# Kernel tuning notes

Measured on AMD Instinct MI355X. Metric: run time of the kernel, lower is better.

## Reference

```python
import jax, jax.numpy as jnp
import numpy as np


def _maxpool2x2(t):
    # t: [B, C, H, W] -> [B, C, H//2, W//2]
    B, C, H, W = t.shape
    return t.reshape(B, C, H // 2, 2, W // 2, 2).max(axis=(3, 5))


def setup_inputs() -> dict:
    key = jax.random.key(0)
    ks = jax.random.split(key, 6)
    B, C, H, W = 2, 64, 128, 128
    x = jax.random.normal(ks[0], (B, C, H, W), dtype=jnp.float32)
    w_theta = jax.random.normal(ks[1], (C // 8, C), dtype=jnp.float32) * 0.05
    w_phi = jax.random.normal(ks[2], (C // 8, C), dtype=jnp.float32) * 0.05
    w_g = jax.random.normal(ks[3], (C // 2, C), dtype=jnp.float32) * 0.05
    w_o = jax.random.normal(ks[4], (C, C // 2), dtype=jnp.float32) * 0.05
    gamma = jnp.ones((1,), dtype=jnp.float32)
    return {"x": x, "w_theta": w_theta, "w_phi": w_phi, "w_g": w_g,
            "w_o": w_o, "gamma": gamma}


def reference(x, w_theta, w_phi, w_g, w_o, gamma):
    B, C, H, W = x.shape
    N = H * W            # query length
    M = (H // 2) * (W // 2)  # downsampled key/value length

    # conv1x1 projections (kernel_size=1 == per-pixel matmul over channels)
    theta = jnp.einsum('bchw,oc->bohw', x, w_theta).reshape(B, C // 8, N)
    phi = jnp.einsum('bchw,oc->bohw', x, w_phi)
    phi = _maxpool2x2(phi).reshape(B, C // 8, M)

    # attention: [B, N, M], unscaled dot product + softmax over keys
    attn = jax.nn.softmax(jnp.einsum('bdn,bdm->bnm', theta, phi), axis=-1)

    g = jnp.einsum('bchw,oc->bohw', x, w_g)
    g = _maxpool2x2(g).reshape(B, C // 2, M)

    attn_g = jnp.einsum('bcm,bnm->bcn', g, attn).reshape(B, C // 2, H, W)
    attn_g = jnp.einsum('bchw,oc->bohw', attn_g, w_o)
    return x + gamma * attn_g
```

## Files before the change

kernel.cpp:

```cpp
#include <hip/hip_runtime.h>

#define BB 2
#define CC 64
#define HH 128
#define WW 128
#define NN (HH*WW)
#define MM ((HH/2)*(WW/2))
#define CV 32
#define LOG2E 1.44269504088896f

typedef __attribute__((ext_vector_type(8))) short bf16x8;
typedef __attribute__((ext_vector_type(4))) float f32x4;
typedef unsigned int uint32;

union U8 { bf16x8 v; uint32 u[4]; };

__device__ __forceinline__ short f2bf(float f) {
    union { float f; unsigned u; } v; v.f = f;
    unsigned u = v.u + 0x7fffu + ((v.u >> 16) & 1u);
    return (short)(u >> 16);
}
__device__ __forceinline__ uint32 pack2bf(float lo, float hi) {
    return (uint32)(unsigned short)f2bf(lo) | ((uint32)(unsigned short)f2bf(hi) << 16);
}
__device__ __forceinline__ uint32 packperm(float lo, float hi) {
    union { float f; uint32 u; } a, b; a.f = lo; b.f = hi;
    return __builtin_amdgcn_perm(b.u, a.u, 0x07060302u);
}
__device__ __forceinline__ void gl_lds16(const short* g, short* l) {
    __builtin_amdgcn_global_load_lds(
        (const __attribute__((address_space(1))) void*)g,
        (__attribute__((address_space(3))) void*)l, 16, 0, 0);
}

__global__ __launch_bounds__(256, 4) void proj_kernel(
    const float* __restrict__ x, const float* __restrict__ wt,
    const float* __restrict__ wp, const float* __restrict__ wg,
    short* __restrict__ Qb, short* __restrict__ Kb, short* __restrict__ Vt)
{
    __shared__ float plds[8192];
    __shared__ float phi_lds[512];
    int tid = threadIdx.x;
    int px = tid & 63, part = tid >> 6;
    int sb = blockIdx.x >> 2, cq = blockIdx.x & 3;
    int b = blockIdx.y, z = blockIdx.z;
    int row = px >> 5, col = cq*32 + (px & 31);
    int n = (2*sb + row)*WW + col;
    int wbase = __builtin_amdgcn_readfirstlane(part*16);

    float xv[16];
    #pragma unroll
    for (int i = 0; i < 16; ++i)
        xv[i] = x[((b*CC + part*16 + i) << 14) + n];

    if (z == 0) {
        float po[16];
        #pragma unroll
        for (int o = 0; o < 8; ++o) {
            float a = 0.f;
            #pragma unroll
            for (int i = 0; i < 16; ++i) a += wt[o*64 + wbase + i]*xv[i];
            po[o] = a;
        }
        #pragma unroll
        for (int o = 0; o < 8; ++o) {
            float a = 0.f;
            #pragma unroll
            for (int i = 0; i < 16; ++i) a += wp[o*64 + wbase + i]*xv[i];
            po[8+o] = a;
        }
        #pragma unroll
        for (int o = 0; o < 16; ++o) plds[(o*4 + part)*64 + px] = po[o];
        __syncthreads();
        int og = tid >> 6;
        float sm[4];
        #pragma unroll
        for (int j = 0; j < 4; ++j) {
            int o = og*4 + j;
            sm[j] = (plds[(o*4+0)*64+px] + plds[(o*4+1)*64+px])
                  + (plds[(o*4+2)*64+px] + plds[(o*4+3)*64+px]);
        }
        if (og < 2) {
            uint2 val;
            val.x = pack2bf(sm[0]*LOG2E, sm[1]*LOG2E);
            val.y = pack2bf(sm[2]*LOG2E, sm[3]*LOG2E);
            ((uint2*)Qb)[(b*NN + n)*2 + og] = val;
        } else {
            #pragma unroll
            for (int j = 0; j < 4; ++j)
                phi_lds[((og-2)*4 + j)*64 + px] = sm[j];
        }
        __syncthreads();
        if (tid < 128) {
            int mm = tid & 15, ch = tid >> 4;
            int p00 = 2*mm, p01 = p00+1, p10 = 32+2*mm, p11 = p10+1;
            float mx = fmaxf(fmaxf(phi_lds[ch*64+p00], phi_lds[ch*64+p01]),
                             fmaxf(phi_lds[ch*64+p10], phi_lds[ch*64+p11]));
            int m = sb*64 + cq*16 + mm;
            Kb[(b*MM + m)*8 + ch] = f2bf(mx);
        }
    } else {
        float po[32];
        #pragma unroll
        for (int o = 0; o < 32; ++o) {
            float a = 0.f;
            #pragma unroll
            for (int i = 0; i < 16; ++i) a += wg[o*64 + wbase + i]*xv[i];
            po[o] = a;
        }
        #pragma unroll
        for (int o = 0; o < 32; ++o) plds[(o*4 + part)*64 + px] = po[o];
        __syncthreads();
        int og = tid >> 6;
        float sm[8];
        #pragma unroll
        for (int j = 0; j < 8; ++j) {
            int o = og*8 + j;
            sm[j] = (plds[(o*4+0)*64+px] + plds[(o*4+1)*64+px])
                  + (plds[(o*4+2)*64+px] + plds[(o*4+3)*64+px]);
        }
        __syncthreads();
        #pragma unroll
        for (int j = 0; j < 8; ++j)
            plds[(og*8 + j)*64 + px] = sm[j];
        __syncthreads();
        int mm = tid & 15, chb = tid >> 4;
        int p00 = 2*mm, p01 = p00+1, p10 = 32+2*mm, p11 = p10+1;
        int w64 = cq*16 + mm;
        int hh = w64 >> 5, w = w64 & 31;
        int slot = ((w >> 2) & 3)*8 + (w & 3) + ((w >> 4) << 2);
        int pos64 = hh*32 + slot;
        #pragma unroll
        for (int j = 0; j < 2; ++j) {
            int ch = chb*2 + j;
            float mx = fmaxf(fmaxf(plds[ch*64+p00], plds[ch*64+p01]),
                             fmaxf(plds[ch*64+p10], plds[ch*64+p11]));
            int colv = (pos64 >> 3) ^ (ch & 7);
            Vt[(b*CV + ch)*MM + sb*64 + colv*8 + (pos64 & 7)] = f2bf(mx);
        }
    }
}

__global__ __launch_bounds__(256, 4) void attn_kernel(
    const short* __restrict__ Qb, const short* __restrict__ Kb,
    const short* __restrict__ Vt, const float* __restrict__ x,
    const float* __restrict__ wo, const float* __restrict__ gamma,
    float* __restrict__ out)
{
    __shared__ short ldsK[2][4][512];
    __shared__ short ldsV[2][4][2048];
    int tid = threadIdx.x;
    int qtr = tid >> 6, lane = tid & 63;
    int quad = lane >> 4, c15 = lane & 15, sw = c15 & 7;
    int blk = blockIdx.x;
    int b = blk >> 9;
    int q0 = (blk & 511)*32;

    const f32x4 zero4 = {0.f, 0.f, 0.f, 0.f};
    bf16x8 zero8 = (bf16x8)0;
    U8 ones; ones.u[0] = ones.u[1] = ones.u[2] = ones.u[3] = 0x3F803F80u;

    bf16x8 bq0 = (quad == 0) ? ((const bf16x8*)Qb)[b*NN + q0 + c15]      : zero8;
    bf16x8 bq1 = (quad == 0) ? ((const bf16x8*)Qb)[b*NN + q0 + 16 + c15] : zero8;

    const short* ksrc  = Kb + (size_t)b*MM*8 + (qtr*1024 + lane)*8;
    const short* vsrcA = Vt + ((size_t)(b*CV + (lane >> 3)))*MM
                       + qtr*1024 + (lane & 7)*8;
    const short* vsrcB = vsrcA + 8*MM;
    const short* vsrcC = vsrcA + 16*MM;
    const short* vsrcD = vsrcA + 24*MM;
    short* kd0 = &ldsK[0][qtr][lane*8];
    short* kd1 = &ldsK[1][qtr][lane*8];
    short* vd0 = &ldsV[0][qtr][lane*8];
    short* vd1 = &ldsV[1][qtr][lane*8];

    {
        gl_lds16(vsrcA, vd0);
        gl_lds16(vsrcB, vd0 + 512);
        gl_lds16(vsrcC, vd0 + 1024);
        gl_lds16(vsrcD, vd0 + 1536);
        gl_lds16(ksrc, kd0);
    }

    f32x4 D0A = zero4, D1A = zero4, DlA = zero4;
    f32x4 D0B = zero4, D1B = zero4, DlB = zero4;

    for (int sc = 0; sc < 16; ++sc) {
        if (sc < 15) {
            int scn = sc + 1;
            short* vd = (scn & 1) ? vd1 : vd0;
            short* kd = (scn & 1) ? kd1 : kd0;
            gl_lds16(vsrcA + scn*64, vd);
            gl_lds16(vsrcB + scn*64, vd + 512);
            gl_lds16(vsrcC + scn*64, vd + 1024);
            gl_lds16(vsrcD + scn*64, vd + 1536);
            gl_lds16(ksrc + scn*512, kd);
            asm volatile("s_waitcnt vmcnt(5)" ::: "memory");
        } else {
            asm volatile("s_waitcnt vmcnt(0)" ::: "memory");
        }
        __builtin_amdgcn_sched_barrier(0);

        const short* bk = (sc & 1) ? &ldsK[1][qtr][0] : &ldsK[0][qtr][0];
        const short* bv = (sc & 1) ? &ldsV[1][qtr][0] : &ldsV[0][qtr][0];
        #pragma unroll
        for (int h = 0; h < 2; ++h) {
            bf16x8 kf0 = *(const bf16x8*)(bk + (h*32 + c15)*8);
            bf16x8 kf1 = *(const bf16x8*)(bk + (h*32 + 16 + c15)*8);
            int col8 = ((h*4 + quad) ^ sw)*8;
            bf16x8 a0 = *(const bf16x8*)(bv + c15*64 + col8);
            bf16x8 a1 = *(const bf16x8*)(bv + (16 + c15)*64 + col8);
            f32x4 s0A = __builtin_amdgcn_mfma_f32_16x16x32_bf16(kf0, bq0, zero4, 0, 0, 0);
            f32x4 s1A = __builtin_amdgcn_mfma_f32_16x16x32_bf16(kf1, bq0, zero4, 0, 0, 0);
            f32x4 s0B = __builtin_amdgcn_mfma_f32_16x16x32_bf16(kf0, bq1, zero4, 0, 0, 0);
            f32x4 s1B = __builtin_amdgcn_mfma_f32_16x16x32_bf16(kf1, bq1, zero4, 0, 0, 0);
            U8 bpA, bpB;
            bpA.u[0] = packperm(__builtin_amdgcn_exp2f(s0A[0]), __builtin_amdgcn_exp2f(s0A[1]));
            bpA.u[1] = packperm(__builtin_amdgcn_exp2f(s0A[2]), __builtin_amdgcn_exp2f(s0A[3]));
            bpA.u[2] = packperm(__builtin_amdgcn_exp2f(s1A[0]), __builtin_amdgcn_exp2f(s1A[1]));
            bpA.u[3] = packperm(__builtin_amdgcn_exp2f(s1A[2]), __builtin_amdgcn_exp2f(s1A[3]));
            bpB.u[0] = packperm(__builtin_amdgcn_exp2f(s0B[0]), __builtin_amdgcn_exp2f(s0B[1]));
            bpB.u[1] = packperm(__builtin_amdgcn_exp2f(s0B[2]), __builtin_amdgcn_exp2f(s0B[3]));
            bpB.u[2] = packperm(__builtin_amdgcn_exp2f(s1B[0]), __builtin_amdgcn_exp2f(s1B[1]));
            bpB.u[3] = packperm(__builtin_amdgcn_exp2f(s1B[2]), __builtin_amdgcn_exp2f(s1B[3]));
            D0A = __builtin_amdgcn_mfma_f32_16x16x32_bf16(a0, bpA.v, D0A, 0, 0, 0);
            D1A = __builtin_amdgcn_mfma_f32_16x16x32_bf16(a1, bpA.v, D1A, 0, 0, 0);
            DlA = __builtin_amdgcn_mfma_f32_16x16x32_bf16(ones.v, bpA.v, DlA, 0, 0, 0);
            D0B = __builtin_amdgcn_mfma_f32_16x16x32_bf16(a0, bpB.v, D0B, 0, 0, 0);
            D1B = __builtin_amdgcn_mfma_f32_16x16x32_bf16(a1, bpB.v, D1B, 0, 0, 0);
            DlB = __builtin_amdgcn_mfma_f32_16x16x32_bf16(ones.v, bpB.v, DlB, 0, 0, 0);
        }
    }

    #pragma unroll
    for (int r = 1; r < 4; ++r) {
        if (qtr == r) {
            float* cA = (float*)&ldsV[0][r][0] + lane*9;
            cA[0]=D0A[0]; cA[1]=D0A[1]; cA[2]=D0A[2]; cA[3]=D0A[3];
            cA[4]=D1A[0]; cA[5]=D1A[1]; cA[6]=D1A[2]; cA[7]=D1A[3];
            cA[8]=DlA[0];
            float* cB = (float*)&ldsV[1][r][0] + lane*9;
            cB[0]=D0B[0]; cB[1]=D0B[1]; cB[2]=D0B[2]; cB[3]=D0B[3];
            cB[4]=D1B[0]; cB[5]=D1B[1]; cB[6]=D1B[2]; cB[7]=D1B[3];
            cB[8]=DlB[0];
        }
        __syncthreads();
        if (qtr == 0) {
            const float* cA = (const float*)&ldsV[0][r][0] + lane*9;
            D0A[0]+=cA[0]; D0A[1]+=cA[1]; D0A[2]+=cA[2]; D0A[3]+=cA[3];
            D1A[0]+=cA[4]; D1A[1]+=cA[5]; D1A[2]+=cA[6]; D1A[3]+=cA[7];
            DlA[0]+=cA[8];
            const float* cB = (const float*)&ldsV[1][r][0] + lane*9;
            D0B[0]+=cB[0]; D0B[1]+=cB[1]; D0B[2]+=cB[2]; D0B[3]+=cB[3];
            D1B[0]+=cB[4]; D1B[1]+=cB[5]; D1B[2]+=cB[6]; D1B[3]+=cB[7];
            DlB[0]+=cB[8];
        }
        __syncthreads();
    }
    if (qtr != 0) return;

    float rlA = 1.0f / DlA[0];
    float rlB = 1.0f / DlB[0];
    U8 ByA, ByB;
    ByA.u[0] = pack2bf(D0A[0]*rlA, D0A[1]*rlA); ByA.u[1] = pack2bf(D0A[2]*rlA, D0A[3]*rlA);
    ByA.u[2] = pack2bf(D1A[0]*rlA, D1A[1]*rlA); ByA.u[3] = pack2bf(D1A[2]*rlA, D1A[3]*rlA);
    ByB.u[0] = pack2bf(D0B[0]*rlB, D0B[1]*rlB); ByB.u[1] = pack2bf(D0B[2]*rlB, D0B[3]*rlB);
    ByB.u[2] = pack2bf(D1B[0]*rlB, D1B[1]*rlB); ByB.u[3] = pack2bf(D1B[2]*rlB, D1B[3]*rlB);

    float gam = gamma[0];
    #pragma unroll
    for (int t = 0; t < 4; ++t) {
        int co = t*16 + c15;
        float4 wlo = *(const float4*)(wo + co*32 + quad*4);
        float4 whi = *(const float4*)(wo + co*32 + 16 + quad*4);
        U8 aw;
        aw.u[0] = pack2bf(wlo.x, wlo.y); aw.u[1] = pack2bf(wlo.z, wlo.w);
        aw.u[2] = pack2bf(whi.x, whi.y); aw.u[3] = pack2bf(whi.z, whi.w);
        f32x4 oA = __builtin_amdgcn_mfma_f32_16x16x32_bf16(aw.v, ByA.v, zero4, 0, 0, 0);
        f32x4 oB = __builtin_amdgcn_mfma_f32_16x16x32_bf16(aw.v, ByB.v, zero4, 0, 0, 0);
        #pragma unroll
        for (int r2 = 0; r2 < 4; ++r2) {
            int co_r = t*16 + quad*4 + r2;
            int base = ((b*CC + co_r) << 14) + q0 + c15;
            out[base]      = x[base]      + gam*oA[r2];
            out[base + 16] = x[base + 16] + gam*oB[r2];
        }
    }
}

extern "C" void kernel_launch(void* const* d_in, const int* in_sizes, int n_in,
                              void* d_out, int out_size, void* d_ws, size_t ws_size,
                              hipStream_t stream) {
    const float* x     = (const float*)d_in[0];
    const float* wt    = (const float*)d_in[1];
    const float* wp    = (const float*)d_in[2];
    const float* wg    = (const float*)d_in[3];
    const float* wo    = (const float*)d_in[4];
    const float* gamma = (const float*)d_in[5];
    float* out = (float*)d_out;

    char* ws = (char*)d_ws;
    short* Qb = (short*)(ws);
    short* Kb = (short*)(ws + 524288);
    short* Vt = (short*)(ws + 655360);

    dim3 g1(256, BB, 2);
    proj_kernel<<<g1, 256, 0, stream>>>(x, wt, wp, wg, Qb, Kb, Vt);
    attn_kernel<<<BB*NN/32, 256, 0, stream>>>(Qb, Kb, Vt, x, wo, gamma, out);
}
```

Before: 100.1 us.

## Deepen V staging to 4-slot ring with finer sub-stages and single-sync reduction

Replaces the double-buffered per-64-key stage loop with a finer 32-key sub-stage pipeline that uses a 4-slot V ring and a 2-slot K buffer per wave, keeping more global-to-LDS loads in flight. It also changes the V layout written by the pool kernel from an XOR-swizzled order to a plain order read as contiguous 16-byte fragments. The cross-wave reduction drops from six block barriers to one, with each wave writing its partials into its own staging region. The risks are LDS bank conflicts under the new unswizzled access pattern and a larger LDS footprint, which could reduce occupancy.

```diff
diff --git a/kernel.cpp b/kernel.cpp
--- a/kernel.cpp
+++ b/kernel.cpp
@@ -135,8 +135,7 @@
             int ch = chb*2 + j;
             float mx = fmaxf(fmaxf(plds[ch*64+p00], plds[ch*64+p01]),
                              fmaxf(plds[ch*64+p10], plds[ch*64+p11]));
-            int colv = (pos64 >> 3) ^ (ch & 7);
-            Vt[(b*CV + ch)*MM + sb*64 + colv*8 + (pos64 & 7)] = f2bf(mx);
+            Vt[(b*CV + ch)*MM + sb*64 + pos64] = f2bf(mx);
         }
     }
 }
@@ -147,11 +146,10 @@
     const float* __restrict__ wo, const float* __restrict__ gamma,
     float* __restrict__ out)
 {
-    __shared__ short ldsK[2][4][512];
-    __shared__ short ldsV[2][4][2048];
+    __shared__ short stage[4][5120];
     int tid = threadIdx.x;
     int qtr = tid >> 6, lane = tid & 63;
-    int quad = lane >> 4, c15 = lane & 15, sw = c15 & 7;
+    int quad = lane >> 4, c15 = lane & 15;
     int blk = blockIdx.x;
     int b = blk >> 9;
     int q0 = (blk & 511)*32;
@@ -163,101 +161,100 @@
     bf16x8 bq0 = (quad == 0) ? ((const bf16x8*)Qb)[b*NN + q0 + c15]      : zero8;
     bf16x8 bq1 = (quad == 0) ? ((const bf16x8*)Qb)[b*NN + q0 + 16 + c15] : zero8;
 
-    const short* ksrc  = Kb + (size_t)b*MM*8 + (qtr*1024 + lane)*8;
-    const short* vsrcA = Vt + ((size_t)(b*CV + (lane >> 3)))*MM
-                       + qtr*1024 + (lane & 7)*8;
-    const short* vsrcB = vsrcA + 8*MM;
-    const short* vsrcC = vsrcA + 16*MM;
-    const short* vsrcD = vsrcA + 24*MM;
-    short* kd0 = &ldsK[0][qtr][lane*8];
-    short* kd1 = &ldsK[1][qtr][lane*8];
-    short* vd0 = &ldsV[0][qtr][lane*8];
-    short* vd1 = &ldsV[1][qtr][lane*8];
-
-    {
-        gl_lds16(vsrcA, vd0);
-        gl_lds16(vsrcB, vd0 + 512);
-        gl_lds16(vsrcC, vd0 + 1024);
-        gl_lds16(vsrcD, vd0 + 1536);
-        gl_lds16(ksrc, kd0);
-    }
+    short* sw_ = &stage[qtr][0];
+    const short* ksrc = Kb + (size_t)b*MM*8 + (qtr*1024 + lane)*8;
+    const short* vsA  = Vt + ((size_t)(b*CV + (lane & 15)))*MM + qtr*1024 + (lane >> 4)*8;
+    const short* vsB  = vsA + 16*MM;
+    short* kdst = sw_ + lane*8;
+    short* vdst = sw_ + 1024 + lane*8;
+
+    gl_lds16(vsA,      vdst);
+    gl_lds16(vsB,      vdst + 512);
+    gl_lds16(ksrc,     kdst);
+    gl_lds16(vsA + 32, vdst + 1024);
+    gl_lds16(vsB + 32, vdst + 1536);
 
     f32x4 D0A = zero4, D1A = zero4, DlA = zero4;
     f32x4 D0B = zero4, D1B = zero4, DlB = zero4;
 
-    for (int sc = 0; sc < 16; ++sc) {
-        if (sc < 15) {
-            int scn = sc + 1;
-            short* vd = (scn & 1) ? vd1 : vd0;
-            short* kd = (scn & 1) ? kd1 : kd0;
-            gl_lds16(vsrcA + scn*64, vd);
-            gl_lds16(vsrcB + scn*64, vd + 512);
-            gl_lds16(vsrcC + scn*64, vd + 1024);
-            gl_lds16(vsrcD + scn*64, vd + 1536);
-            gl_lds16(ksrc + scn*512, kd);
-            asm volatile("s_waitcnt vmcnt(5)" ::: "memory");
-        } else {
-            asm volatile("s_waitcnt vmcnt(0)" ::: "memory");
-        }
-        __builtin_amdgcn_sched_barrier(0);
-
-        const short* bk = (sc & 1) ? &ldsK[1][qtr][0] : &ldsK[0][qtr][0];
-        const short* bv = (sc & 1) ? &ldsV[1][qtr][0] : &ldsV[0][qtr][0];
-        #pragma unroll
-        for (int h = 0; h < 2; ++h) {
-            bf16x8 kf0 = *(const bf16x8*)(bk + (h*32 + c15)*8);
-            bf16x8 kf1 = *(const bf16x8*)(bk + (h*32 + 16 + c15)*8);
-            int col8 = ((h*4 + quad) ^ sw)*8;
-            bf16x8 a0 = *(const bf16x8*)(bv + c15*64 + col8);
-            bf16x8 a1 = *(const bf16x8*)(bv + (16 + c15)*64 + col8);
-            f32x4 s0A = __builtin_amdgcn_mfma_f32_16x16x32_bf16(kf0, bq0, zero4, 0, 0, 0);
-            f32x4 s1A = __builtin_amdgcn_mfma_f32_16x16x32_bf16(kf1, bq0, zero4, 0, 0, 0);
-            f32x4 s0B = __builtin_amdgcn_mfma_f32_16x16x32_bf16(kf0, bq1, zero4, 0, 0, 0);
-            f32x4 s1B = __builtin_amdgcn_mfma_f32_16x16x32_bf16(kf1, bq1, zero4, 0, 0, 0);
-            U8 bpA, bpB;
-            bpA.u[0] = packperm(__builtin_amdgcn_exp2f(s0A[0]), __builtin_amdgcn_exp2f(s0A[1]));
-            bpA.u[1] = packperm(__builtin_amdgcn_exp2f(s0A[2]), __builtin_amdgcn_exp2f(s0A[3]));
-            bpA.u[2] = packperm(__builtin_amdgcn_exp2f(s1A[0]), __builtin_amdgcn_exp2f(s1A[1]));
-            bpA.u[3] = packperm(__builtin_amdgcn_exp2f(s1A[2]), __builtin_amdgcn_exp2f(s1A[3]));
-            bpB.u[0] = packperm(__builtin_amdgcn_exp2f(s0B[0]), __builtin_amdgcn_exp2f(s0B[1]));
-            bpB.u[1] = packperm(__builtin_amdgcn_exp2f(s0B[2]), __builtin_amdgcn_exp2f(s0B[3]));
-            bpB.u[2] = packperm(__builtin_amdgcn_exp2f(s1B[0]), __builtin_amdgcn_exp2f(s1B[1]));
-            bpB.u[3] = packperm(__builtin_amdgcn_exp2f(s1B[2]), __builtin_amdgcn_exp2f(s1B[3]));
-            D0A = __builtin_amdgcn_mfma_f32_16x16x32_bf16(a0, bpA.v, D0A, 0, 0, 0);
-            D1A = __builtin_amdgcn_mfma_f32_16x16x32_bf16(a1, bpA.v, D1A, 0, 0, 0);
-            DlA = __builtin_amdgcn_mfma_f32_16x16x32_bf16(ones.v, bpA.v, DlA, 0, 0, 0);
-            D0B = __builtin_amdgcn_mfma_f32_16x16x32_bf16(a0, bpB.v, D0B, 0, 0, 0);
-            D1B = __builtin_amdgcn_mfma_f32_16x16x32_bf16(a1, bpB.v, D1B, 0, 0, 0);
-            DlB = __builtin_amdgcn_mfma_f32_16x16x32_bf16(ones.v, bpB.v, DlB, 0, 0, 0);
-        }
-    }
+#define SUBSTAGE(T, VB, KB, H, IV, IK, WN)                                      \
+    {                                                                           \
+        if (IV) {                                                               \
+            gl_lds16(vsA + ((T)+2)*32, vdst + ((((VB)+2)&3))*1024);             \
+            gl_lds16(vsB + ((T)+2)*32, vdst + ((((VB)+2)&3))*1024 + 512);       \
+        }                                                                       \
+        if (IK) {                                                               \
+            gl_lds16(ksrc + ((((T)>>1)+1))*512, kdst + ((((((T)>>1)+1))&1))*512);\
+        }                                                                       \
+        asm volatile("s_waitcnt vmcnt(" #WN ")" ::: "memory");                  \
+        __builtin_amdgcn_sched_barrier(0);                                      \
+        const short* bk = sw_ + (KB)*512;                                       \
+        const short* bv = sw_ + 1024 + (VB)*1024;                               \
+        bf16x8 kf0 = *(const bf16x8*)(bk + ((H)*32 + c15)*8);                   \
+        bf16x8 kf1 = *(const bf16x8*)(bk + ((H)*32 + 16 + c15)*8);              \
+        bf16x8 a0  = *(const bf16x8*)(bv + quad*128 + c15*8);                   \
+        bf16x8 a1  = *(const bf16x8*)(bv + 512 + quad*128 + c15*8);             \
+        f32x4 s0A = __builtin_amdgcn_mfma_f32_16x16x32_bf16(kf0, bq0, zero4, 0, 0, 0); \
+        f32x4 s1A = __builtin_amdgcn_mfma_f32_16x16x32_bf16(kf1, bq0, zero4, 0, 0, 0); \
+        f32x4 s0B = __builtin_amdgcn_mfma_f32_16x16x32_bf16(kf0, bq1, zero4, 0, 0, 0); \
+        f32x4 s1B = __builtin_amdgcn_mfma_f32_16x16x32_bf16(kf1, bq1, zero4, 0, 0, 0); \
+        U8 bpA, bpB;                                                            \
+        bpA.u[0] = packperm(__builtin_amdgcn_exp2f(s0A[0]), __builtin_amdgcn_exp2f(s0A[1])); \
+        bpA.u[1] = packperm(__builtin_amdgcn_exp2f(s0A[2]), __builtin_amdgcn_exp2f(s0A[3])); \
+        bpA.u[2] = packperm(__builtin_amdgcn_exp2f(s1A[0]), __builtin_amdgcn_exp2f(s1A[1])); \
+        bpA.u[3] = packperm(__builtin_amdgcn_exp2f(s1A[2]), __builtin_amdgcn_exp2f(s1A[3])); \
+        bpB.u[0] = packperm(__builtin_amdgcn_exp2f(s0B[0]), __builtin_amdgcn_exp2f(s0B[1])); \
+        bpB.u[1] = packperm(__builtin_amdgcn_exp2f(s0B[2]), __builtin_amdgcn_exp2f(s0B[3])); \
+        bpB.u[2] = packperm(__builtin_amdgcn_exp2f(s1B[0]), __builtin_amdgcn_exp2f(s1B[1])); \
+        bpB.u[3] = packperm(__builtin_amdgcn_exp2f(s1B[2]), __builtin_amdgcn_exp2f(s1B[3])); \
+        D0A = __builtin_amdgcn_mfma_f32_16x16x32_bf16(a0, bpA.v, D0A, 0, 0, 0); \
+        D1A = __builtin_amdgcn_mfma_f32_16x16x32_bf16(a1, bpA.v, D1A, 0, 0, 0); \
+        DlA = __builtin_amdgcn_mfma_f32_16x16x32_bf16(ones.v, bpA.v, DlA, 0, 0, 0); \
+        D0B = __builtin_amdgcn_mfma_f32_16x16x32_bf16(a0, bpB.v, D0B, 0, 0, 0); \
+        D1B = __builtin_amdgcn_mfma_f32_16x16x32_bf16(a1, bpB.v, D1B, 0, 0, 0); \
+        DlB = __builtin_amdgcn_mfma_f32_16x16x32_bf16(ones.v, bpB.v, DlB, 0, 0, 0); \
+    }
+
+    #pragma unroll 1
+    for (int tp = 0; tp < 7; ++tp) {
+        int T0 = 4*tp;
+        SUBSTAGE(T0+0, 0, 0, 0, 1, 1, 5)
+        SUBSTAGE(T0+1, 1, 0, 1, 1, 0, 5)
+        SUBSTAGE(T0+2, 2, 1, 0, 1, 1, 5)
+        SUBSTAGE(T0+3, 3, 1, 1, 1, 0, 5)
+    }
+    SUBSTAGE(28, 0, 0, 0, 1, 1, 5)
+    SUBSTAGE(29, 1, 0, 1, 1, 0, 5)
+    SUBSTAGE(30, 2, 1, 0, 0, 0, 2)
+    SUBSTAGE(31, 3, 1, 1, 0, 0, 0)
+#undef SUBSTAGE
+
+    if (qtr != 0) {
+        float* cb = (float*)sw_;
+        float* cA = cb + lane*9;
+        cA[0]=D0A[0]; cA[1]=D0A[1]; cA[2]=D0A[2]; cA[3]=D0A[3];
+        cA[4]=D1A[0]; cA[5]=D1A[1]; cA[6]=D1A[2]; cA[7]=D1A[3];
+        cA[8]=DlA[0];
+        float* cB = cb + 576 + lane*9;
+        cB[0]=D0B[0]; cB[1]=D0B[1]; cB[2]=D0B[2]; cB[3]=D0B[3];
+        cB[4]=D1B[0]; cB[5]=D1B[1]; cB[6]=D1B[2]; cB[7]=D1B[3];
+        cB[8]=DlB[0];
+    }
+    __syncthreads();
+    if (qtr != 0) return;
 
     #pragma unroll
     for (int r = 1; r < 4; ++r) {
-        if (qtr == r) {
-            float* cA = (float*)&ldsV[0][r][0] + lane*9;
-            cA[0]=D0A[0]; cA[1]=D0A[1]; cA[2]=D0A[2]; cA[3]=D0A[3];
-            cA[4]=D1A[0]; cA[5]=D1A[1]; cA[6]=D1A[2]; cA[7]=D1A[3];
-            cA[8]=DlA[0];
-            float* cB = (float*)&ldsV[1][r][0] + lane*9;
-            cB[0]=D0B[0]; cB[1]=D0B[1]; cB[2]=D0B[2]; cB[3]=D0B[3];
-            cB[4]=D1B[0]; cB[5]=D1B[1]; cB[6]=D1B[2]; cB[7]=D1B[3];
-            cB[8]=DlB[0];
-        }
-        __syncthreads();
-        if (qtr == 0) {
-            const float* cA = (const float*)&ldsV[0][r][0] + lane*9;
-            D0A[0]+=cA[0]; D0A[1]+=cA[1]; D0A[2]+=cA[2]; D0A[3]+=cA[3];
-            D1A[0]+=cA[4]; D1A[1]+=cA[5]; D1A[2]+=cA[6]; D1A[3]+=cA[7];
-            DlA[0]+=cA[8];
-            const float* cB = (const float*)&ldsV[1][r][0] + lane*9;
-            D0B[0]+=cB[0]; D0B[1]+=cB[1]; D0B[2]+=cB[2]; D0B[3]+=cB[3];
-            D1B[0]+=cB[4]; D1B[1]+=cB[5]; D1B[2]+=cB[6]; D1B[3]+=cB[7];
-            DlB[0]+=cB[8];
-        }
-        __syncthreads();
-    }
-    if (qtr != 0) return;
+        const float* cb = (const float*)&stage[r][0];
+        const float* cA = cb + lane*9;
+        D0A[0]+=cA[0]; D0A[1]+=cA[1]; D0A[2]+=cA[2]; D0A[3]+=cA[3];
+        D1A[0]+=cA[4]; D1A[1]+=cA[5]; D1A[2]+=cA[6]; D1A[3]+=cA[7];
+        DlA[0]+=cA[8];
+        const float* cB = cb + 576 + lane*9;
+        D0B[0]+=cB[0]; D0B[1]+=cB[1]; D0B[2]+=cB[2]; D0B[3]+=cB[3];
+        D1B[0]+=cB[4]; D1B[1]+=cB[5]; D1B[2]+=cB[6]; D1B[3]+=cB[7];
+        DlB[0]+=cB[8];
+    }
 
     float rlA = 1.0f / DlA[0];
     float rlB = 1.0f / DlB[0];
```

Result: slower. 112.1 us (+12.0%).

## Software-pipeline QK MFMAs one half-chunk ahead of exp and PV accumulation

Applied to the files above, without the earlier changes.

Restructures the attention inner loop so the QK^T MFMAs and LDS fragment loads for the next half-chunk are issued before the exp2/pack and PV MFMAs of the previous half-chunk. A prologue prefetches two chunks and an epilogue drains the pipeline. The loop is unrolled by 2, and the per-iteration sched_barrier is removed. The aim is to hide MFMA latency and transcendental work behind each other, at the cost of more live registers.

```diff
diff --git a/kernel.cpp b/kernel.cpp
--- a/kernel.cpp
+++ b/kernel.cpp
@@ -174,63 +174,107 @@
     short* vd0 = &ldsV[0][qtr][lane*8];
     short* vd1 = &ldsV[1][qtr][lane*8];
 
-    {
-        gl_lds16(vsrcA, vd0);
-        gl_lds16(vsrcB, vd0 + 512);
-        gl_lds16(vsrcC, vd0 + 1024);
-        gl_lds16(vsrcD, vd0 + 1536);
-        gl_lds16(ksrc, kd0);
-    }
+    gl_lds16(vsrcA, vd0);       gl_lds16(vsrcB, vd0 + 512);
+    gl_lds16(vsrcC, vd0 + 1024); gl_lds16(vsrcD, vd0 + 1536);
+    gl_lds16(ksrc, kd0);
+    gl_lds16(vsrcA + 64, vd1);       gl_lds16(vsrcB + 64, vd1 + 512);
+    gl_lds16(vsrcC + 64, vd1 + 1024); gl_lds16(vsrcD + 64, vd1 + 1536);
+    gl_lds16(ksrc + 512, kd1);
+    asm volatile("s_waitcnt vmcnt(5)" ::: "memory");
 
     f32x4 D0A = zero4, D1A = zero4, DlA = zero4;
     f32x4 D0B = zero4, D1B = zero4, DlB = zero4;
 
-    for (int sc = 0; sc < 16; ++sc) {
-        if (sc < 15) {
-            int scn = sc + 1;
-            short* vd = (scn & 1) ? vd1 : vd0;
-            short* kd = (scn & 1) ? kd1 : kd0;
-            gl_lds16(vsrcA + scn*64, vd);
-            gl_lds16(vsrcB + scn*64, vd + 512);
-            gl_lds16(vsrcC + scn*64, vd + 1024);
-            gl_lds16(vsrcD + scn*64, vd + 1536);
-            gl_lds16(ksrc + scn*512, kd);
-            asm volatile("s_waitcnt vmcnt(5)" ::: "memory");
-        } else {
-            asm volatile("s_waitcnt vmcnt(0)" ::: "memory");
-        }
-        __builtin_amdgcn_sched_barrier(0);
+    f32x4 pA0, pA1, pB0, pB1;
+    bf16x8 pa0, pa1;
+
+#define LOADQK(bk, bv, H, cA0, cA1, cB0, cB1, ca0, ca1)                         \
+    bf16x8 kf0_##H = *(const bf16x8*)((bk) + ((H)*32 + c15)*8);                 \
+    bf16x8 kf1_##H = *(const bf16x8*)((bk) + ((H)*32 + 16 + c15)*8);            \
+    bf16x8 ca0 = *(const bf16x8*)((bv) + c15*64 + (((H)*4 + quad) ^ sw)*8);     \
+    bf16x8 ca1 = *(const bf16x8*)((bv) + (16 + c15)*64 + (((H)*4 + quad) ^ sw)*8);\
+    f32x4 cA0 = __builtin_amdgcn_mfma_f32_16x16x32_bf16(kf0_##H, bq0, zero4, 0, 0, 0); \
+    f32x4 cA1 = __builtin_amdgcn_mfma_f32_16x16x32_bf16(kf1_##H, bq0, zero4, 0, 0, 0); \
+    f32x4 cB0 = __builtin_amdgcn_mfma_f32_16x16x32_bf16(kf0_##H, bq1, zero4, 0, 0, 0); \
+    f32x4 cB1 = __builtin_amdgcn_mfma_f32_16x16x32_bf16(kf1_##H, bq1, zero4, 0, 0, 0);
+
+#define SMPV()                                                                  \
+    {                                                                           \
+        U8 bpA, bpB;                                                            \
+        bpA.u[0] = packperm(__builtin_amdgcn_exp2f(pA0[0]), __builtin_amdgcn_exp2f(pA0[1])); \
+        bpA.u[1] = packperm(__builtin_amdgcn_exp2f(pA0[2]), __builtin_amdgcn_exp2f(pA0[3])); \
+        bpA.u[2] = packperm(__builtin_amdgcn_exp2f(pA1[0]), __builtin_amdgcn_exp2f(pA1[1])); \
+        bpA.u[3] = packperm(__builtin_amdgcn_exp2f(pA1[2]), __builtin_amdgcn_exp2f(pA1[3])); \
+        bpB.u[0] = packperm(__builtin_amdgcn_exp2f(pB0[0]), __builtin_amdgcn_exp2f(pB0[1])); \
+        bpB.u[1] = packperm(__builtin_amdgcn_exp2f(pB0[2]), __builtin_amdgcn_exp2f(pB0[3])); \
+        bpB.u[2] = packperm(__builtin_amdgcn_exp2f(pB1[0]), __builtin_amdgcn_exp2f(pB1[1])); \
+        bpB.u[3] = packperm(__builtin_amdgcn_exp2f(pB1[2]), __builtin_amdgcn_exp2f(pB1[3])); \
+        D0A = __builtin_amdgcn_mfma_f32_16x16x32_bf16(pa0, bpA.v, D0A, 0, 0, 0);\
+        D1A = __builtin_amdgcn_mfma_f32_16x16x32_bf16(pa1, bpA.v, D1A, 0, 0, 0);\
+        DlA = __builtin_amdgcn_mfma_f32_16x16x32_bf16(ones.v, bpA.v, DlA, 0, 0, 0);\
+        D0B = __builtin_amdgcn_mfma_f32_16x16x32_bf16(pa0, bpB.v, D0B, 0, 0, 0);\
+        D1B = __builtin_amdgcn_mfma_f32_16x16x32_bf16(pa1, bpB.v, D1B, 0, 0, 0);\
+        DlB = __builtin_amdgcn_mfma_f32_16x16x32_bf16(ones.v, bpB.v, DlB, 0, 0, 0);\
+    }
+
+#define ROT(cA0, cA1, cB0, cB1, ca0, ca1)                                       \
+    pA0 = cA0; pA1 = cA1; pB0 = cB0; pB1 = cB1; pa0 = ca0; pa1 = ca1;
+
+    {
+        const short* bk = &ldsK[0][qtr][0];
+        const short* bv = &ldsV[0][qtr][0];
+        LOADQK(bk, bv, 0, xA0, xA1, xB0, xB1, xa0, xa1)
+        ROT(xA0, xA1, xB0, xB1, xa0, xa1)
+        LOADQK(bk, bv, 1, yA0, yA1, yB0, yB1, ya0, ya1)
+        SMPV()
+        ROT(yA0, yA1, yB0, yB1, ya0, ya1)
+    }
+
+    #pragma unroll 2
+    for (int sc = 1; sc < 15; ++sc) {
+        int scn = sc + 1;
+        short* vd = (scn & 1) ? vd1 : vd0;
+        short* kd = (scn & 1) ? kd1 : kd0;
+        gl_lds16(vsrcA + scn*64, vd);
+        gl_lds16(vsrcB + scn*64, vd + 512);
+        gl_lds16(vsrcC + scn*64, vd + 1024);
+        gl_lds16(vsrcD + scn*64, vd + 1536);
+        gl_lds16(ksrc + scn*512, kd);
+        asm volatile("s_waitcnt vmcnt(5)" ::: "memory");
 
         const short* bk = (sc & 1) ? &ldsK[1][qtr][0] : &ldsK[0][qtr][0];
         const short* bv = (sc & 1) ? &ldsV[1][qtr][0] : &ldsV[0][qtr][0];
-        #pragma unroll
-        for (int h = 0; h < 2; ++h) {
-            bf16x8 kf0 = *(const bf16x8*)(bk + (h*32 + c15)*8);
-            bf16x8 kf1 = *(const bf16x8*)(bk + (h*32 + 16 + c15)*8);
-            int col8 = ((h*4 + quad) ^ sw)*8;
-            bf16x8 a0 = *(const bf16x8*)(bv + c15*64 + col8);
-            bf16x8 a1 = *(const bf16x8*)(bv + (16 + c15)*64 + col8);
-            f32x4 s0A = __builtin_amdgcn_mfma_f32_16x16x32_bf16(kf0, bq0, zero4, 0, 0, 0);
-            f32x4 s1A = __builtin_amdgcn_mfma_f32_16x16x32_bf16(kf1, bq0, zero4, 0, 0, 0);
-            f32x4 s0B = __builtin_amdgcn_mfma_f32_16x16x32_bf16(kf0, bq1, zero4, 0, 0, 0);
-            f32x4 s1B = __builtin_amdgcn_mfma_f32_16x16x32_bf16(kf1, bq1, zero4, 0, 0, 0);
-            U8 bpA, bpB;
-            bpA.u[0] = packperm(__builtin_amdgcn_exp2f(s0A[0]), __builtin_amdgcn_exp2f(s0A[1]));
-            bpA.u[1] = packperm(__builtin_amdgcn_exp2f(s0A[2]), __builtin_amdgcn_exp2f(s0A[3]));
-            bpA.u[2] = packperm(__builtin_amdgcn_exp2f(s1A[0]), __builtin_amdgcn_exp2f(s1A[1]));
-            bpA.u[3] = packperm(__builtin_amdgcn_exp2f(s1A[2]), __builtin_amdgcn_exp2f(s1A[3]));
-            bpB.u[0] = packperm(__builtin_amdgcn_exp2f(s0B[0]), __builtin_amdgcn_exp2f(s0B[1]));
-            bpB.u[1] = packperm(__builtin_amdgcn_exp2f(s0B[2]), __builtin_amdgcn_exp2f(s0B[3]));
-            bpB.u[2] = packperm(__builtin_amdgcn_exp2f(s1B[0]), __builtin_amdgcn_exp2f(s1B[1]));
-            bpB.u[3] = packperm(__builtin_amdgcn_exp2f(s1B[2]), __builtin_amdgcn_exp2f(s1B[3]));
-            D0A = __builtin_amdgcn_mfma_f32_16x16x32_bf16(a0, bpA.v, D0A, 0, 0, 0);
-            D1A = __builtin_amdgcn_mfma_f32_16x16x32_bf16(a1, bpA.v, D1A, 0, 0, 0);
-            DlA = __builtin_amdgcn_mfma_f32_16x16x32_bf16(ones.v, bpA.v, DlA, 0, 0, 0);
-            D0B = __builtin_amdgcn_mfma_f32_16x16x32_bf16(a0, bpB.v, D0B, 0, 0, 0);
-            D1B = __builtin_amdgcn_mfma_f32_16x16x32_bf16(a1, bpB.v, D1B, 0, 0, 0);
-            DlB = __builtin_amdgcn_mfma_f32_16x16x32_bf16(ones.v, bpB.v, DlB, 0, 0, 0);
-        }
-    }
+        {
+            LOADQK(bk, bv, 0, xA0, xA1, xB0, xB1, xa0, xa1)
+            SMPV()
+            ROT(xA0, xA1, xB0, xB1, xa0, xa1)
+        }
+        {
+            LOADQK(bk, bv, 1, yA0, yA1, yB0, yB1, ya0, ya1)
+            SMPV()
+            ROT(yA0, yA1, yB0, yB1, ya0, ya1)
+        }
+    }
+
+    {
+        asm volatile("s_waitcnt vmcnt(0)" ::: "memory");
+        const short* bk = &ldsK[1][qtr][0];
+        const short* bv = &ldsV[1][qtr][0];
+        {
+            LOADQK(bk, bv, 0, xA0, xA1, xB0, xB1, xa0, xa1)
+            SMPV()
+            ROT(xA0, xA1, xB0, xB1, xa0, xa1)
+        }
+        {
+            LOADQK(bk, bv, 1, yA0, yA1, yB0, yB1, ya0, ya1)
+            SMPV()
+            ROT(yA0, yA1, yB0, yB1, ya0, ya1)
+        }
+        SMPV()
+    }
+#undef LOADQK
+#undef SMPV
+#undef ROT
 
     #pragma unroll
     for (int r = 1; r < 4; ++r) {
```

Result: no change. 99.68 us (-0.4%).

## Split attention key range across eight waves with smaller per-wave tiles

Applied to the files above, without the earlier changes.

The attention kernel now launches 512 threads, and each of eight waves streams its own 512-key slice. Each wave processes a 32-key chunk per iteration instead of two 32-key halves, and the V layout drops the XOR swizzle in favour of a plain layout that matches the new LDS fragment reads. The cross-wave partial-sum reduction becomes a single barrier followed by wave 0 summing seven slots. This is meant to add latency hiding and parallelism and to cut barrier rounds, at the cost of more reduction work in wave 0, possible LDS bank conflicts from the unswizzled layout, and higher per-block resource use.

```diff
diff --git a/kernel.cpp b/kernel.cpp
--- a/kernel.cpp
+++ b/kernel.cpp
@@ -135,23 +135,21 @@
             int ch = chb*2 + j;
             float mx = fmaxf(fmaxf(plds[ch*64+p00], plds[ch*64+p01]),
                              fmaxf(plds[ch*64+p10], plds[ch*64+p11]));
-            int colv = (pos64 >> 3) ^ (ch & 7);
-            Vt[(b*CV + ch)*MM + sb*64 + colv*8 + (pos64 & 7)] = f2bf(mx);
-        }
-    }
-}
-
-__global__ __launch_bounds__(256, 4) void attn_kernel(
+            Vt[(b*CV + ch)*MM + sb*64 + pos64] = f2bf(mx);
+        }
+    }
+}
+
+__global__ __launch_bounds__(512, 8) void attn_kernel(
     const short* __restrict__ Qb, const short* __restrict__ Kb,
     const short* __restrict__ Vt, const float* __restrict__ x,
     const float* __restrict__ wo, const float* __restrict__ gamma,
     float* __restrict__ out)
 {
-    __shared__ short ldsK[2][4][512];
-    __shared__ short ldsV[2][4][2048];
+    __shared__ short stage[8][2560];
     int tid = threadIdx.x;
-    int qtr = tid >> 6, lane = tid & 63;
-    int quad = lane >> 4, c15 = lane & 15, sw = c15 & 7;
+    int wv = tid >> 6, lane = tid & 63;
+    int quad = lane >> 4, c15 = lane & 15;
     int blk = blockIdx.x;
     int b = blk >> 9;
     int q0 = (blk & 511)*32;
@@ -163,23 +161,18 @@
     bf16x8 bq0 = (quad == 0) ? ((const bf16x8*)Qb)[b*NN + q0 + c15]      : zero8;
     bf16x8 bq1 = (quad == 0) ? ((const bf16x8*)Qb)[b*NN + q0 + 16 + c15] : zero8;
 
-    const short* ksrc  = Kb + (size_t)b*MM*8 + (qtr*1024 + lane)*8;
-    const short* vsrcA = Vt + ((size_t)(b*CV + (lane >> 3)))*MM
-                       + qtr*1024 + (lane & 7)*8;
-    const short* vsrcB = vsrcA + 8*MM;
-    const short* vsrcC = vsrcA + 16*MM;
-    const short* vsrcD = vsrcA + 24*MM;
-    short* kd0 = &ldsK[0][qtr][lane*8];
-    short* kd1 = &ldsK[1][qtr][lane*8];
-    short* vd0 = &ldsV[0][qtr][lane*8];
-    short* vd1 = &ldsV[1][qtr][lane*8];
+    short* sw_ = &stage[wv][0];
+    const short* ksrc = Kb + ((size_t)b*MM + wv*512 + lane)*8;
+    const short* vsrc = Vt + ((size_t)(b*CV + (lane & 15)))*MM + wv*512 + (lane >> 4)*8;
+    short* kd0 = sw_ + lane*8;
+    short* kd1 = sw_ + 256 + lane*8;
+    short* vd0 = sw_ + 512 + lane*8;
+    short* vd1 = sw_ + 1536 + lane*8;
 
     {
-        gl_lds16(vsrcA, vd0);
-        gl_lds16(vsrcB, vd0 + 512);
-        gl_lds16(vsrcC, vd0 + 1024);
-        gl_lds16(vsrcD, vd0 + 1536);
-        gl_lds16(ksrc, kd0);
+        gl_lds16(vsrc,         vd0);
+        gl_lds16(vsrc + 16*MM, vd0 + 512);
+        if (lane < 32) gl_lds16(ksrc, kd0);
     }
 
     f32x4 D0A = zero4, D1A = zero4, DlA = zero4;
@@ -190,74 +183,68 @@
             int scn = sc + 1;
             short* vd = (scn & 1) ? vd1 : vd0;
             short* kd = (scn & 1) ? kd1 : kd0;
-            gl_lds16(vsrcA + scn*64, vd);
-            gl_lds16(vsrcB + scn*64, vd + 512);
-            gl_lds16(vsrcC + scn*64, vd + 1024);
-            gl_lds16(vsrcD + scn*64, vd + 1536);
-            gl_lds16(ksrc + scn*512, kd);
-            asm volatile("s_waitcnt vmcnt(5)" ::: "memory");
+            gl_lds16(vsrc + scn*32,         vd);
+            gl_lds16(vsrc + 16*MM + scn*32, vd + 512);
+            if (lane < 32) gl_lds16(ksrc + scn*256, kd);
+            asm volatile("s_waitcnt vmcnt(3)" ::: "memory");
         } else {
             asm volatile("s_waitcnt vmcnt(0)" ::: "memory");
         }
         __builtin_amdgcn_sched_barrier(0);
 
-        const short* bk = (sc & 1) ? &ldsK[1][qtr][0] : &ldsK[0][qtr][0];
-        const short* bv = (sc & 1) ? &ldsV[1][qtr][0] : &ldsV[0][qtr][0];
-        #pragma unroll
-        for (int h = 0; h < 2; ++h) {
-            bf16x8 kf0 = *(const bf16x8*)(bk + (h*32 + c15)*8);
-            bf16x8 kf1 = *(const bf16x8*)(bk + (h*32 + 16 + c15)*8);
-            int col8 = ((h*4 + quad) ^ sw)*8;
-            bf16x8 a0 = *(const bf16x8*)(bv + c15*64 + col8);
-            bf16x8 a1 = *(const bf16x8*)(bv + (16 + c15)*64 + col8);
-            f32x4 s0A = __builtin_amdgcn_mfma_f32_16x16x32_bf16(kf0, bq0, zero4, 0, 0, 0);
-            f32x4 s1A = __builtin_amdgcn_mfma_f32_16x16x32_bf16(kf1, bq0, zero4, 0, 0, 0);
-            f32x4 s0B = __builtin_amdgcn_mfma_f32_16x16x32_bf16(kf0, bq1, zero4, 0, 0, 0);
-            f32x4 s1B = __builtin_amdgcn_mfma_f32_16x16x32_bf16(kf1, bq1, zero4, 0, 0, 0);
-            U8 bpA, bpB;
-            bpA.u[0] = packperm(__builtin_amdgcn_exp2f(s0A[0]), __builtin_amdgcn_exp2f(s0A[1]));
-            bpA.u[1] = packperm(__builtin_amdgcn_exp2f(s0A[2]), __builtin_amdgcn_exp2f(s0A[3]));
-            bpA.u[2] = packperm(__builtin_amdgcn_exp2f(s1A[0]), __builtin_amdgcn_exp2f(s1A[1]));
-            bpA.u[3] = packperm(__builtin_amdgcn_exp2f(s1A[2]), __builtin_amdgcn_exp2f(s1A[3]));
-            bpB.u[0] = packperm(__builtin_amdgcn_exp2f(s0B[0]), __builtin_amdgcn_exp2f(s0B[1]));
-            bpB.u[1] = packperm(__builtin_amdgcn_exp2f(s0B[2]), __builtin_amdgcn_exp2f(s0B[3]));
-            bpB.u[2] = packperm(__builtin_amdgcn_exp2f(s1B[0]), __builtin_amdgcn_exp2f(s1B[1]));
-            bpB.u[3] = packperm(__builtin_amdgcn_exp2f(s1B[2]), __builtin_amdgcn_exp2f(s1B[3]));
-            D0A = __builtin_amdgcn_mfma_f32_16x16x32_bf16(a0, bpA.v, D0A, 0, 0, 0);
-            D1A = __builtin_amdgcn_mfma_f32_16x16x32_bf16(a1, bpA.v, D1A, 0, 0, 0);
-            DlA = __builtin_amdgcn_mfma_f32_16x16x32_bf16(ones.v, bpA.v, DlA, 0, 0, 0);
-            D0B = __builtin_amdgcn_mfma_f32_16x16x32_bf16(a0, bpB.v, D0B, 0, 0, 0);
-            D1B = __builtin_amdgcn_mfma_f32_16x16x32_bf16(a1, bpB.v, D1B, 0, 0, 0);
-            DlB = __builtin_amdgcn_mfma_f32_16x16x32_bf16(ones.v, bpB.v, DlB, 0, 0, 0);
-        }
-    }
+        const short* bk = sw_ + (sc & 1)*256;
+        const short* bv = sw_ + 512 + (sc & 1)*1024;
+        bf16x8 kf0 = *(const bf16x8*)(bk + c15*8);
+        bf16x8 kf1 = *(const bf16x8*)(bk + (16 + c15)*8);
+        bf16x8 a0 = *(const bf16x8*)(bv + quad*128 + c15*8);
+        bf16x8 a1 = *(const bf16x8*)(bv + 512 + quad*128 + c15*8);
+        f32x4 s0A = __builtin_amdgcn_mfma_f32_16x16x32_bf16(kf0, bq0, zero4, 0, 0, 0);
+        f32x4 s1A = __builtin_amdgcn_mfma_f32_16x16x32_bf16(kf1, bq0, zero4, 0, 0, 0);
+        f32x4 s0B = __builtin_amdgcn_mfma_f32_16x16x32_bf16(kf0, bq1, zero4, 0, 0, 0);
+        f32x4 s1B = __builtin_amdgcn_mfma_f32_16x16x32_bf16(kf1, bq1, zero4, 0, 0, 0);
+        U8 bpA, bpB;
+        bpA.u[0] = packperm(__builtin_amdgcn_exp2f(s0A[0]), __builtin_amdgcn_exp2f(s0A[1]));
+        bpA.u[1] = packperm(__builtin_amdgcn_exp2f(s0A[2]), __builtin_amdgcn_exp2f(s0A[3]));
+        bpA.u[2] = packperm(__builtin_amdgcn_exp2f(s1A[0]), __builtin_amdgcn_exp2f(s1A[1]));
+        bpA.u[3] = packperm(__builtin_amdgcn_exp2f(s1A[2]), __builtin_amdgcn_exp2f(s1A[3]));
+        bpB.u[0] = packperm(__builtin_amdgcn_exp2f(s0B[0]), __builtin_amdgcn_exp2f(s0B[1]));
+        bpB.u[1] = packperm(__builtin_amdgcn_exp2f(s0B[2]), __builtin_amdgcn_exp2f(s0B[3]));
+        bpB.u[2] = packperm(__builtin_amdgcn_exp2f(s1B[0]), __builtin_amdgcn_exp2f(s1B[1]));
+        bpB.u[3] = packperm(__builtin_amdgcn_exp2f(s1B[2]), __builtin_amdgcn_exp2f(s1B[3]));
+        D0A = __builtin_amdgcn_mfma_f32_16x16x32_bf16(a0, bpA.v, D0A, 0, 0, 0);
+        D1A = __builtin_amdgcn_mfma_f32_16x16x32_bf16(a1, bpA.v, D1A, 0, 0, 0);
+        DlA = __builtin_amdgcn_mfma_f32_16x16x32_bf16(ones.v, bpA.v, DlA, 0, 0, 0);
+        D0B = __builtin_amdgcn_mfma_f32_16x16x32_bf16(a0, bpB.v, D0B, 0, 0, 0);
+        D1B = __builtin_amdgcn_mfma_f32_16x16x32_bf16(a1, bpB.v, D1B, 0, 0, 0);
+        DlB = __builtin_amdgcn_mfma_f32_16x16x32_bf16(ones.v, bpB.v, DlB, 0, 0, 0);
+    }
+
+    if (wv != 0) {
+        float* cb = (float*)sw_;
+        float* cA = cb + lane*9;
+        cA[0]=D0A[0]; cA[1]=D0A[1]; cA[2]=D0A[2]; cA[3]=D0A[3];
+        cA[4]=D1A[0]; cA[5]=D1A[1]; cA[6]=D1A[2]; cA[7]=D1A[3];
+        cA[8]=DlA[0];
+        float* cB = cb + 576 + lane*9;
+        cB[0]=D0B[0]; cB[1]=D0B[1]; cB[2]=D0B[2]; cB[3]=D0B[3];
+        cB[4]=D1B[0]; cB[5]=D1B[1]; cB[6]=D1B[2]; cB[7]=D1B[3];
+        cB[8]=DlB[0];
+    }
+    __syncthreads();
+    if (wv != 0) return;
 
     #pragma unroll
-    for (int r = 1; r < 4; ++r) {
-        if (qtr == r) {
-            float* cA = (float*)&ldsV[0][r][0] + lane*9;
-            cA[0]=D0A[0]; cA[1]=D0A[1]; cA[2]=D0A[2]; cA[3]=D0A[3];
-            cA[4]=D1A[0]; cA[5]=D1A[1]; cA[6]=D1A[2]; cA[7]=D1A[3];
-            cA[8]=DlA[0];
-            float* cB = (float*)&ldsV[1][r][0] + lane*9;
-            cB[0]=D0B[0]; cB[1]=D0B[1]; cB[2]=D0B[2]; cB[3]=D0B[3];
-            cB[4]=D1B[0]; cB[5]=D1B[1]; cB[6]=D1B[2]; cB[7]=D1B[3];
-            cB[8]=DlB[0];
-        }
-        __syncthreads();
-        if (qtr == 0) {
-            const float* cA = (const float*)&ldsV[0][r][0] + lane*9;
-            D0A[0]+=cA[0]; D0A[1]+=cA[1]; D0A[2]+=cA[2]; D0A[3]+=cA[3];
-            D1A[0]+=cA[4]; D1A[1]+=cA[5]; D1A[2]+=cA[6]; D1A[3]+=cA[7];
-            DlA[0]+=cA[8];
-            const float* cB = (const float*)&ldsV[1][r][0] + lane*9;
-            D0B[0]+=cB[0]; D0B[1]+=cB[1]; D0B[2]+=cB[2]; D0B[3]+=cB[3];
-            D1B[0]+=cB[4]; D1B[1]+=cB[5]; D1B[2]+=cB[6]; D1B[3]+=cB[7];
-            DlB[0]+=cB[8];
-        }
-        __syncthreads();
-    }
-    if (qtr != 0) return;
+    for (int r = 1; r < 8; ++r) {
+        const float* cb = (const float*)&stage[r][0];
+        const float* cA = cb + lane*9;
+        D0A[0]+=cA[0]; D0A[1]+=cA[1]; D0A[2]+=cA[2]; D0A[3]+=cA[3];
+        D1A[0]+=cA[4]; D1A[1]+=cA[5]; D1A[2]+=cA[6]; D1A[3]+=cA[7];
+        DlA[0]+=cA[8];
+        const float* cB = cb + 576 + lane*9;
+        D0B[0]+=cB[0]; D0B[1]+=cB[1]; D0B[2]+=cB[2]; D0B[3]+=cB[3];
+        D1B[0]+=cB[4]; D1B[1]+=cB[5]; D1B[2]+=cB[6]; D1B[3]+=cB[7];
+        DlB[0]+=cB[8];
+    }
 
     float rlA = 1.0f / DlA[0];
     float rlB = 1.0f / DlB[0];
@@ -306,5 +293,5 @@
 
     dim3 g1(256, BB, 2);
     proj_kernel<<<g1, 256, 0, stream>>>(x, wt, wp, wg, Qb, Kb, Vt);
-    attn_kernel<<<BB*NN/32, 256, 0, stream>>>(Qb, Kb, Vt, x, wo, gamma, out);
-}
+    attn_kernel<<<BB*NN/32, 512, 0, stream>>>(Qb, Kb, Vt, x, wo, gamma, out);
+}
```

New measurement: 144.9 us. +44.8%, slower.
